# Kernel tuning notes

Hardware: AMD Instinct MI355X
Metric: run time of the kernel (lower is better)

Reference implementation:

```python
import jax, jax.numpy as jnp
import numpy as np
import math

B, S, E, H = 2, 2048, 1024, 16


def setup_inputs() -> dict:
    key = jax.random.key(0)
    ks = jax.random.split(key, 9)
    std = 0.02
    return {
        "x": jax.random.normal(ks[0], (B, S, E), dtype=jnp.float32),
        "Wq": jax.random.normal(ks[1], (E, E), dtype=jnp.float32) * std,
        "bq": jnp.zeros((E,), dtype=jnp.float32),
        "Wk": jax.random.normal(ks[2], (E, E), dtype=jnp.float32) * std,
        "bk": jnp.zeros((E,), dtype=jnp.float32),
        "Wv": jax.random.normal(ks[3], (E, E), dtype=jnp.float32) * std,
        "bv": jnp.zeros((E,), dtype=jnp.float32),
        "Wfc": jax.random.normal(ks[4], (E, E), dtype=jnp.float32) * std,
        "bfc": jnp.zeros((E,), dtype=jnp.float32),
        "n_head": H,
    }


def reference(x, Wq, bq, Wk, bk, Wv, bv, Wfc, bfc, n_head):
    Bn, Sn, En = x.shape
    Hd = En // n_head  # head_dim
    # torch Linear: y = x @ W.T + b
    def proj(W, b):
        return (x @ W.T + b).reshape(Bn, Sn, n_head, Hd).transpose(0, 2, 1, 3)  # [B,H,S,D]
    q = proj(Wq, bq)
    k = proj(Wk, bk)
    v = proj(Wv, bv)
    scores = jnp.einsum('bhqd,bhkd->bhqk', q, k) / math.sqrt(Hd)  # [B,H,S,S]
    # ALiBi: slopes_h = 2^{-(h+1)}; alibi[h,i,j] = -slope_h * (i - j)
    slopes = 2.0 ** (-jnp.arange(1, n_head + 1, dtype=jnp.float32))  # [H]
    pos = jnp.arange(Sn, dtype=jnp.float32)
    rel = pos[:, None] - pos[None, :]  # [S,S], memory_pos - context_pos
    alibi = -slopes[:, None, None] * rel  # [H,S,S]
    scores = scores + alibi[None]
    weights = jax.nn.softmax(scores, axis=-1)  # [B,H,S,S]
    out = jnp.einsum('bhqk,bhkd->bqhd', weights, v).reshape(Bn, Sn, En)
    out = out @ Wfc.T + bfc
    return (out, weights)
```

## Files before the change

### kernel.cpp

```cpp
#include <hip/hip_runtime.h>
#include <hip/hip_bf16.h>
#include <cstdint>
#include <cstddef>

#define BB 2
#define SS 2048
#define EE 1024
#define HH 16
#define MM (BB*SS)

typedef __bf16 bf16;
typedef __bf16 bf16x8 __attribute__((ext_vector_type(8)));
typedef float f32x4 __attribute__((ext_vector_type(4)));

#define GLD16(gsrc, ldst) \
  __builtin_amdgcn_global_load_lds((const __attribute__((address_space(1))) void*)(gsrc), \
                                   (__attribute__((address_space(3))) void*)(ldst), 16, 0, 0)

#define VMWAIT(N) do { asm volatile("s_waitcnt vmcnt(" #N ")" ::: "memory"); \
                       __builtin_amdgcn_sched_barrier(0); } while (0)
#define XBAR() do { __builtin_amdgcn_s_barrier(); \
                    __builtin_amdgcn_sched_barrier(0); } while (0)

__global__ __launch_bounds__(256) void cvt_f32_bf16(const float* __restrict__ src,
                                                    bf16* __restrict__ dst, int n) {
    int i = (blockIdx.x * 256 + threadIdx.x) * 8;
    if (i >= n) return;
    float4 a = *(const float4*)(src + i);
    float4 b = *(const float4*)(src + i + 4);
    bf16 o[8] = {(bf16)a.x,(bf16)a.y,(bf16)a.z,(bf16)a.w,
                 (bf16)b.x,(bf16)b.y,(bf16)b.z,(bf16)b.w};
    *(uint4*)(dst + i) = *(uint4*)o;
}

__global__ __launch_bounds__(256) void cvt4(const float* __restrict__ a, const float* __restrict__ b,
                                            const float* __restrict__ c, const float* __restrict__ d,
                                            bf16* __restrict__ oa, bf16* __restrict__ ob,
                                            bf16* __restrict__ oc, bf16* __restrict__ od) {
    int sel = blockIdx.y;
    const float* s = sel == 0 ? a : sel == 1 ? b : sel == 2 ? c : d;
    bf16* o       = sel == 0 ? oa : sel == 1 ? ob : sel == 2 ? oc : od;
    int i = (blockIdx.x * 256 + threadIdx.x) * 8;
    float4 x = *(const float4*)(s + i);
    float4 y = *(const float4*)(s + i + 4);
    bf16 t[8] = {(bf16)x.x,(bf16)x.y,(bf16)x.z,(bf16)x.w,
                 (bf16)y.x,(bf16)y.y,(bf16)y.z,(bf16)y.w};
    *(uint4*)(o + i) = *(uint4*)t;
}

template<int MODE>
__global__ __launch_bounds__(256) void gemm128(const bf16* __restrict__ A,
                                               const bf16* __restrict__ W0,
                                               const bf16* __restrict__ W1,
                                               const bf16* __restrict__ W2,
                                               const float* __restrict__ b0,
                                               const float* __restrict__ b1,
                                               const float* __restrict__ b2,
                                               void* __restrict__ o0,
                                               void* __restrict__ o1,
                                               void* __restrict__ o2) {
    __shared__ bf16 Al[128*64];
    __shared__ bf16 Bl[128*64];
    const int t = threadIdx.x;
    const int wsel = blockIdx.x >> 3;
    const int n0 = (blockIdx.x & 7) * 128;
    const int m0 = blockIdx.y * 128;
    const bf16* W  = wsel == 0 ? W0 : wsel == 1 ? W1 : W2;
    const float* bias = wsel == 0 ? b0 : wsel == 1 ? b1 : b2;
    void* outp = wsel == 0 ? o0 : wsel == 1 ? o1 : o2;

    const int w = t >> 6, lane = t & 63, lg = lane >> 4, li = lane & 15;
    const int wr = w >> 1, wc = w & 1;
    f32x4 acc[4][4] = {};

    for (int k0 = 0; k0 < 1024; k0 += 64) {
        __syncthreads();
        #pragma unroll
        for (int i = 0; i < 4; ++i) {
            int f = i * 256 + t;
            int row = f >> 3, c = (f & 7) * 8;
            GLD16(A + (size_t)(m0 + row) * 1024 + k0 + c, Al + f * 8);
            GLD16(W + (size_t)(n0 + row) * 1024 + k0 + c, Bl + f * 8);
        }
        __syncthreads();
        #pragma unroll
        for (int ks = 0; ks < 2; ++ks) {
            bf16x8 af[4], bf_[4];
            #pragma unroll
            for (int m = 0; m < 4; ++m)
                af[m] = *(const bf16x8*)&Al[(wr*64 + m*16 + li)*64 + ks*32 + lg*8];
            #pragma unroll
            for (int n = 0; n < 4; ++n)
                bf_[n] = *(const bf16x8*)&Bl[(wc*64 + n*16 + li)*64 + ks*32 + lg*8];
            #pragma unroll
            for (int m = 0; m < 4; ++m)
                #pragma unroll
                for (int n = 0; n < 4; ++n)
                    acc[m][n] = __builtin_amdgcn_mfma_f32_16x16x32_bf16(af[m], bf_[n], acc[m][n], 0,0,0);
        }
    }
    #pragma unroll
    for (int m = 0; m < 4; ++m)
      #pragma unroll
      for (int n = 0; n < 4; ++n)
        #pragma unroll
        for (int r = 0; r < 4; ++r) {
            int row = m0 + wr*64 + m*16 + lg*4 + r;
            int col = n0 + wc*64 + n*16 + li;
            float v = acc[m][n][r] + bias[col];
            if (MODE == 0) {
                int b = row >> 11, s = row & (SS-1);
                int h = col >> 6, d = col & 63;
                ((bf16*)outp)[(((size_t)(b*HH + h)*SS + s) << 6) + d] = (bf16)v;
            } else {
                ((float*)outp)[(size_t)row*1024 + col] = v;
            }
        }
}

__global__ __launch_bounds__(256) void transpose_v(const bf16* __restrict__ V,
                                                   bf16* __restrict__ Vt) {
    __shared__ bf16 L[64][72];
    const int bh = blockIdx.y, s0 = blockIdx.x * 64, t = threadIdx.x;
    for (int id = t; id < 512; id += 256) {
        int row = id >> 3, c = id & 7;
        *(uint4*)&L[row][c*8] = *(const uint4*)&V[((size_t)bh*SS + s0 + row)*64 + c*8];
    }
    __syncthreads();
    for (int id = t; id < 512; id += 256) {
        int d = id >> 3, c = id & 7;
        bf16 tmp[8];
        #pragma unroll
        for (int jj = 0; jj < 8; ++jj) tmp[jj] = L[c*8 + jj][d];
        *(uint4*)&Vt[((size_t)bh*64 + d)*SS + s0 + c*8] = *(uint4*)tmp;
    }
}

__global__ __launch_bounds__(256) void attn_kernel(const bf16* __restrict__ Q,
                                                   const bf16* __restrict__ Kk,
                                                   const bf16* __restrict__ Vt,
                                                   float* __restrict__ wout,
                                                   bf16* __restrict__ aout) {
    __shared__ bf16 ring[4][64*64];
    __shared__ float Lred[2][64];

    const int lin = blockIdx.x + (int)(gridDim.x * blockIdx.y);
    const int nl  = (lin & 7) * 128 + (lin >> 3);
    const int qt = nl & 31, bh = nl >> 5;

    const int b = bh >> 4, h = bh & 15;
    const int q0 = qt * 64;
    const int t = threadIdx.x, w = t >> 6, lane = t & 63, lg = lane >> 4, li = lane & 15;
    const int jh = w & 1, qh = w >> 1;
    const float slope = exp2f(-(float)(h + 1));
    const size_t kvbase = (size_t)bh * SS * 64;
    const size_t vtbase = (size_t)bh * 64 * SS;
    const float L2E = 1.4426950408889634f;
    const float K1 = 0.125f * L2E;
    const float C  = slope * L2E;
    const float C64 = C * 64.f;

    bf16x8 aq[2][2];
    #pragma unroll
    for (int cbq = 0; cbq < 2; ++cbq) {
        const bf16* qptr = Q + kvbase + (size_t)(q0 + qh*32 + cbq*16 + li) * 64;
        aq[cbq][0] = *(const bf16x8*)(qptr + lg*8);
        aq[cbq][1] = *(const bf16x8*)(qptr + 32 + lg*8);
    }

    const int swz = (li & 7) << 4;

    #define STAGE_K(J0, DST) do {                                              \
        _Pragma("unroll")                                                      \
        for (int i_ = 0; i_ < 2; ++i_) {                                       \
            int f_ = i_*256 + t; int row_ = f_ >> 3, c_ = f_ & 7;              \
            GLD16(Kk + kvbase + (size_t)((J0) + row_)*64 + (c_ ^ (row_ & 7))*8,\
                  (DST) + f_*8);                                               \
        } } while (0)
    #define STAGE_V(J0, DST) do {                                              \
        _Pragma("unroll")                                                      \
        for (int i_ = 0; i_ < 2; ++i_) {                                       \
            int f_ = i_*256 + t; int row_ = f_ >> 3, c_ = f_ & 7;              \
            GLD16(Vt + vtbase + (size_t)row_*SS + (J0) + (c_ ^ (row_ & 7))*8,  \
                  (DST) + f_*8);                                               \
        } } while (0)

    float cj[2][4];
    #pragma unroll
    for (int jt = 0; jt < 2; ++jt)
        #pragma unroll
        for (int r = 0; r < 4; ++r)
            cj[jt][r] = C * (float)(jh*32 + jt*16 + lg*4 + r - (SS-1));
    float lp[2] = {0.f, 0.f};

    STAGE_K(0,  &ring[0][0]);
    STAGE_K(64, &ring[1][0]);
    VMWAIT(2);
    XBAR();
    for (int kt = 0; kt < 32; ++kt) {
        if (kt + 2 < 32) STAGE_K((kt+2)*64, &ring[(kt+2) & 3][0]);
        const char* Ksb = (const char*)&ring[kt & 3][0];
        bf16x8 ak[2][2];
        #pragma unroll
        for (int jt = 0; jt < 2; ++jt) {
            int row = jh*32 + jt*16 + li;
            ak[jt][0] = *(const bf16x8*)(Ksb + row*128 + ((     lg*16) ^ swz));
            ak[jt][1] = *(const bf16x8*)(Ksb + row*128 + ((64 + lg*16) ^ swz));
        }
        f32x4 sc[2][2] = {};
        __builtin_amdgcn_s_setprio(1);
        #pragma unroll
        for (int jt = 0; jt < 2; ++jt)
            #pragma unroll
            for (int cbq = 0; cbq < 2; ++cbq) {
                sc[jt][cbq] = __builtin_amdgcn_mfma_f32_16x16x32_bf16(ak[jt][0], aq[cbq][0], sc[jt][cbq], 0,0,0);
                sc[jt][cbq] = __builtin_amdgcn_mfma_f32_16x16x32_bf16(ak[jt][1], aq[cbq][1], sc[jt][cbq], 0,0,0);
            }
        __builtin_amdgcn_s_setprio(0);
        #pragma unroll
        for (int jt = 0; jt < 2; ++jt) {
            #pragma unroll
            for (int cbq = 0; cbq < 2; ++cbq)
                #pragma unroll
                for (int r = 0; r < 4; ++r)
                    lp[cbq] += __builtin_amdgcn_exp2f(fmaf(sc[jt][cbq][r], K1, cj[jt][r]));
            #pragma unroll
            for (int r = 0; r < 4; ++r) cj[jt][r] += C64;
        }
        if (kt < 30) { VMWAIT(2); } else { VMWAIT(0); }
        XBAR();
    }
    #pragma unroll
    for (int cbq = 0; cbq < 2; ++cbq) {
        lp[cbq] += __shfl_xor(lp[cbq], 16);
        lp[cbq] += __shfl_xor(lp[cbq], 32);
    }
    if (lg == 0) {
        Lred[jh][qh*32 + li]      = lp[0];
        Lred[jh][qh*32 + 16 + li] = lp[1];
    }
    STAGE_K(0, &ring[0][0]);
    STAGE_V(0, &ring[2][0]);
    asm volatile("s_waitcnt vmcnt(0) lgkmcnt(0)" ::: "memory");
    __builtin_amdgcn_sched_barrier(0);
    XBAR();
    float lgl[2];
    #pragma unroll
    for (int cbq = 0; cbq < 2; ++cbq) {
        int qi = qh*32 + cbq*16 + li;
        lgl[cbq] = __builtin_amdgcn_logf(Lred[0][qi] + Lred[1][qi]);
    }
    float ecr[2][2][4];
    #pragma unroll
    for (int jt = 0; jt < 2; ++jt)
        #pragma unroll
        for (int cbq = 0; cbq < 2; ++cbq)
            #pragma unroll
            for (int r = 0; r < 4; ++r)
                ecr[jt][cbq][r] = C * (float)(jh*32 + jt*16 + lg*4 + r - (SS-1)) - lgl[cbq];

    f32x4 acc[2][4] = {};
    float* wrow0 = wout + ((size_t)bh*SS + q0 + qh*32 +      li) * SS;
    float* wrow1 = wout + ((size_t)bh*SS + q0 + qh*32 + 16 + li) * SS;

    for (int kt = 0; kt < 32; ++kt) {
        const int cur = kt & 1;
        const int j0 = kt * 64;
        if (kt + 1 < 32) {
            STAGE_K(j0 + 64, &ring[cur ^ 1][0]);
            STAGE_V(j0 + 64, &ring[2 + (cur ^ 1)][0]);
        }
        const char* Ksb = (const char*)&ring[cur][0];
        const char* Vsb = (const char*)&ring[2 + cur][0];
        bf16x8 ak[2][2];
        #pragma unroll
        for (int jt = 0; jt < 2; ++jt) {
            int row = jh*32 + jt*16 + li;
            ak[jt][0] = *(const bf16x8*)(Ksb + row*128 + ((     lg*16) ^ swz));
            ak[jt][1] = *(const bf16x8*)(Ksb + row*128 + ((64 + lg*16) ^ swz));
        }
        f32x4 sc[2][2] = {};
        __builtin_amdgcn_s_setprio(1);
        #pragma unroll
        for (int jt = 0; jt < 2; ++jt)
            #pragma unroll
            for (int cbq = 0; cbq < 2; ++cbq) {
                sc[jt][cbq] = __builtin_amdgcn_mfma_f32_16x16x32_bf16(ak[jt][0], aq[cbq][0], sc[jt][cbq], 0,0,0);
                sc[jt][cbq] = __builtin_amdgcn_mfma_f32_16x16x32_bf16(ak[jt][1], aq[cbq][1], sc[jt][cbq], 0,0,0);
            }
        __builtin_amdgcn_s_setprio(0);
        f32x4 wv[2][2];
        #pragma unroll
        for (int jt = 0; jt < 2; ++jt)
            #pragma unroll
            for (int cbq = 0; cbq < 2; ++cbq) {
                f32x4 v;
                v[0] = __builtin_amdgcn_exp2f(fmaf(sc[jt][cbq][0], K1, ecr[jt][cbq][0]));
                v[1] = __builtin_amdgcn_exp2f(fmaf(sc[jt][cbq][1], K1, ecr[jt][cbq][1]));
                v[2] = __builtin_amdgcn_exp2f(fmaf(sc[jt][cbq][2], K1, ecr[jt][cbq][2]));
                v[3] = __builtin_amdgcn_exp2f(fmaf(sc[jt][cbq][3], K1, ecr[jt][cbq][3]));
                wv[jt][cbq] = v;
                float* wr = (cbq == 0 ? wrow0 : wrow1);
                __builtin_nontemporal_store(v, (f32x4*)&wr[j0 + jh*32 + jt*16 + lg*4]);
                ecr[jt][cbq][0] += C64; ecr[jt][cbq][1] += C64;
                ecr[jt][cbq][2] += C64; ecr[jt][cbq][3] += C64;
            }
        bf16x8 pa[2];
        #pragma unroll
        for (int cbq = 0; cbq < 2; ++cbq) {
            bf16x8 p;
            p[0] = (bf16)wv[0][cbq][0]; p[1] = (bf16)wv[0][cbq][1];
            p[2] = (bf16)wv[0][cbq][2]; p[3] = (bf16)wv[0][cbq][3];
            p[4] = (bf16)wv[1][cbq][0]; p[5] = (bf16)wv[1][cbq][1];
            p[6] = (bf16)wv[1][cbq][2]; p[7] = (bf16)wv[1][cbq][3];
            pa[cbq] = p;
        }
        bf16x8 vb[4];
        #pragma unroll
        for (int d0 = 0; d0 < 4; ++d0) {
            int row = d0*16 + li;
            uint2 u0 = *(const uint2*)(Vsb + row*128 + ((jh*64      + lg*8) ^ swz));
            uint2 u1 = *(const uint2*)(Vsb + row*128 + ((jh*64 + 32 + lg*8) ^ swz));
            uint4 uu = {u0.x, u0.y, u1.x, u1.y};
            vb[d0] = __builtin_bit_cast(bf16x8, uu);
        }
        __builtin_amdgcn_s_setprio(1);
        #pragma unroll
        for (int cbq = 0; cbq < 2; ++cbq)
            #pragma unroll
            for (int d0 = 0; d0 < 4; ++d0)
                acc[cbq][d0] = __builtin_amdgcn_mfma_f32_16x16x32_bf16(pa[cbq], vb[d0], acc[cbq][d0], 0,0,0);
        __builtin_amdgcn_s_setprio(0);
        VMWAIT(4);
        XBAR();
    }

    bf16* Obuf = &ring[0][0];
    #pragma unroll
    for (int cbq = 0; cbq < 2; ++cbq)
        #pragma unroll
        for (int d0 = 0; d0 < 4; ++d0)
            #pragma unroll
            for (int r = 0; r < 4; ++r)
                Obuf[jh*4096 + (qh*32 + cbq*16 + lg*4 + r)*64 + d0*16 + li] =
                    (bf16)acc[cbq][d0][r];
    __syncthreads();
    {
        int q = t >> 2, dc = (t & 3) << 4;
        const bf16* o0 = Obuf +        q*64 + dc;
        const bf16* o1 = Obuf + 4096 + q*64 + dc;
        bf16x8 a0 = *(const bf16x8*)(o0),     a1 = *(const bf16x8*)(o0 + 8);
        bf16x8 b0 = *(const bf16x8*)(o1),     b1 = *(const bf16x8*)(o1 + 8);
        bf16 ov[16];
        #pragma unroll
        for (int e = 0; e < 8; ++e) {
            ov[e]     = (bf16)((float)a0[e] + (float)b0[e]);
            ov[8 + e] = (bf16)((float)a1[e] + (float)b1[e]);
        }
        bf16* dst = aout + ((size_t)(b*SS + q0 + q))*EE + h*64 + dc;
        *(uint4*)(dst)     = *(uint4*)(ov);
        *(uint4*)(dst + 8) = *(uint4*)(ov + 8);
    }
    #undef STAGE_K
    #undef STAGE_V
}

extern "C" void kernel_launch(void* const* d_in, const int* in_sizes, int n_in,
                              void* d_out, int out_size, void* d_ws, size_t ws_size,
                              hipStream_t stream) {
    const float* x   = (const float*)d_in[0];
    const float* Wq  = (const float*)d_in[1];
    const float* bq  = (const float*)d_in[2];
    const float* Wk  = (const float*)d_in[3];
    const float* bk  = (const float*)d_in[4];
    const float* Wv  = (const float*)d_in[5];
    const float* bv  = (const float*)d_in[6];
    const float* Wfc = (const float*)d_in[7];
    const float* bfc = (const float*)d_in[8];

    char* ws = (char*)d_ws;
    const size_t MB = 1024u*1024u;
    bf16* xb  = (bf16*)(ws + 0);
    bf16* wqb = (bf16*)(ws + 8*MB);
    bf16* wkb = (bf16*)(ws + 10*MB);
    bf16* wvb = (bf16*)(ws + 12*MB);
    bf16* wfb = (bf16*)(ws + 14*MB);
    bf16* Qb  = (bf16*)(ws + 16*MB);
    bf16* Kb  = (bf16*)(ws + 24*MB);
    bf16* Vb  = (bf16*)(ws + 32*MB);
    bf16* Vtb = (bf16*)(ws + 40*MB);
    bf16* Ab  = (bf16*)(ws + 48*MB);

    float* outp = (float*)d_out;
    float* wout = outp + (size_t)BB*SS*EE;

    cvt_f32_bf16<<<dim3(4194304/8/256), 256, 0, stream>>>(x, xb, 4194304);
    cvt4<<<dim3(512, 4), 256, 0, stream>>>(Wq, Wk, Wv, Wfc, wqb, wkb, wvb, wfb);

    gemm128<0><<<dim3(24, 32), 256, 0, stream>>>(xb, wqb, wkb, wvb, bq, bk, bv, Qb, Kb, Vb);

    transpose_v<<<dim3(SS/64, BB*HH), 256, 0, stream>>>(Vb, Vtb);

    attn_kernel<<<dim3(32, 32), 256, 0, stream>>>(Qb, Kb, Vtb, wout, Ab);

    gemm128<1><<<dim3(8, 32), 256, 0, stream>>>(Ab, wfb, wfb, wfb, bfc, bfc, bfc, d_out, d_out, d_out);
}
```

Baseline: 299.8 us.

## Split attention into PV pass with deferred normalization and separate weights-writing kernel

The single attention kernel did two passes over K: first to compute softmax denominators, then to compute normalized weights, store them and accumulate PV. Now attn1 does one pass that accumulates unnormalized PV together with the row sums, then rescales the output by the inverse sum and writes the log-sum to a workspace buffer. A new weights_kernel recomputes QK^T from global K, reads the log-sum and streams the normalized weights matrix, split over twice as many blocks. This removes the dedicated row-sum pass from the PV kernel but still recomputes QK^T for the weights output and adds a kernel launch. It also drops the custom vmcnt waits in favour of plain __syncthreads, and the log-sum buffer reuses the xb workspace region.

Result: slower. 341.4 us (+13.9%).

```diff
diff --git a/kernel.cpp b/kernel.cpp
--- a/kernel.cpp
+++ b/kernel.cpp
@@ -16,11 +16,6 @@
 #define GLD16(gsrc, ldst) \
   __builtin_amdgcn_global_load_lds((const __attribute__((address_space(1))) void*)(gsrc), \
                                    (__attribute__((address_space(3))) void*)(ldst), 16, 0, 0)
-
-#define VMWAIT(N) do { asm volatile("s_waitcnt vmcnt(" #N ")" ::: "memory"); \
-                       __builtin_amdgcn_sched_barrier(0); } while (0)
-#define XBAR() do { __builtin_amdgcn_s_barrier(); \
-                    __builtin_amdgcn_sched_barrier(0); } while (0)
 
 __global__ __launch_bounds__(256) void cvt_f32_bf16(const float* __restrict__ src,
                                                     bf16* __restrict__ dst, int n) {
@@ -136,11 +131,11 @@
     }
 }
 
-__global__ __launch_bounds__(256) void attn_kernel(const bf16* __restrict__ Q,
-                                                   const bf16* __restrict__ Kk,
-                                                   const bf16* __restrict__ Vt,
-                                                   float* __restrict__ wout,
-                                                   bf16* __restrict__ aout) {
+__global__ __launch_bounds__(256) void attn1_kernel(const bf16* __restrict__ Q,
+                                                    const bf16* __restrict__ Kk,
+                                                    const bf16* __restrict__ Vt,
+                                                    float* __restrict__ Lbuf,
+                                                    bf16* __restrict__ aout) {
     __shared__ bf16 ring[4][64*64];
     __shared__ float Lred[2][64];
 
@@ -167,7 +162,6 @@
         aq[cbq][0] = *(const bf16x8*)(qptr + lg*8);
         aq[cbq][1] = *(const bf16x8*)(qptr + 32 + lg*8);
     }
-
     const int swz = (li & 7) << 4;
 
     #define STAGE_K(J0, DST) do {                                              \
@@ -192,77 +186,11 @@
         for (int r = 0; r < 4; ++r)
             cj[jt][r] = C * (float)(jh*32 + jt*16 + lg*4 + r - (SS-1));
     float lp[2] = {0.f, 0.f};
-
-    STAGE_K(0,  &ring[0][0]);
-    STAGE_K(64, &ring[1][0]);
-    VMWAIT(2);
-    XBAR();
-    for (int kt = 0; kt < 32; ++kt) {
-        if (kt + 2 < 32) STAGE_K((kt+2)*64, &ring[(kt+2) & 3][0]);
-        const char* Ksb = (const char*)&ring[kt & 3][0];
-        bf16x8 ak[2][2];
-        #pragma unroll
-        for (int jt = 0; jt < 2; ++jt) {
-            int row = jh*32 + jt*16 + li;
-            ak[jt][0] = *(const bf16x8*)(Ksb + row*128 + ((     lg*16) ^ swz));
-            ak[jt][1] = *(const bf16x8*)(Ksb + row*128 + ((64 + lg*16) ^ swz));
-        }
-        f32x4 sc[2][2] = {};
-        __builtin_amdgcn_s_setprio(1);
-        #pragma unroll
-        for (int jt = 0; jt < 2; ++jt)
-            #pragma unroll
-            for (int cbq = 0; cbq < 2; ++cbq) {
-                sc[jt][cbq] = __builtin_amdgcn_mfma_f32_16x16x32_bf16(ak[jt][0], aq[cbq][0], sc[jt][cbq], 0,0,0);
-                sc[jt][cbq] = __builtin_amdgcn_mfma_f32_16x16x32_bf16(ak[jt][1], aq[cbq][1], sc[jt][cbq], 0,0,0);
-            }
-        __builtin_amdgcn_s_setprio(0);
-        #pragma unroll
-        for (int jt = 0; jt < 2; ++jt) {
-            #pragma unroll
-            for (int cbq = 0; cbq < 2; ++cbq)
-                #pragma unroll
-                for (int r = 0; r < 4; ++r)
-                    lp[cbq] += __builtin_amdgcn_exp2f(fmaf(sc[jt][cbq][r], K1, cj[jt][r]));
-            #pragma unroll
-            for (int r = 0; r < 4; ++r) cj[jt][r] += C64;
-        }
-        if (kt < 30) { VMWAIT(2); } else { VMWAIT(0); }
-        XBAR();
-    }
-    #pragma unroll
-    for (int cbq = 0; cbq < 2; ++cbq) {
-        lp[cbq] += __shfl_xor(lp[cbq], 16);
-        lp[cbq] += __shfl_xor(lp[cbq], 32);
-    }
-    if (lg == 0) {
-        Lred[jh][qh*32 + li]      = lp[0];
-        Lred[jh][qh*32 + 16 + li] = lp[1];
-    }
+    f32x4 acc[2][4] = {};
+
     STAGE_K(0, &ring[0][0]);
     STAGE_V(0, &ring[2][0]);
-    asm volatile("s_waitcnt vmcnt(0) lgkmcnt(0)" ::: "memory");
-    __builtin_amdgcn_sched_barrier(0);
-    XBAR();
-    float lgl[2];
-    #pragma unroll
-    for (int cbq = 0; cbq < 2; ++cbq) {
-        int qi = qh*32 + cbq*16 + li;
-        lgl[cbq] = __builtin_amdgcn_logf(Lred[0][qi] + Lred[1][qi]);
-    }
-    float ecr[2][2][4];
-    #pragma unroll
-    for (int jt = 0; jt < 2; ++jt)
-        #pragma unroll
-        for (int cbq = 0; cbq < 2; ++cbq)
-            #pragma unroll
-            for (int r = 0; r < 4; ++r)
-                ecr[jt][cbq][r] = C * (float)(jh*32 + jt*16 + lg*4 + r - (SS-1)) - lgl[cbq];
-
-    f32x4 acc[2][4] = {};
-    float* wrow0 = wout + ((size_t)bh*SS + q0 + qh*32 +      li) * SS;
-    float* wrow1 = wout + ((size_t)bh*SS + q0 + qh*32 + 16 + li) * SS;
-
+    __syncthreads();
     for (int kt = 0; kt < 32; ++kt) {
         const int cur = kt & 1;
         const int j0 = kt * 64;
@@ -291,20 +219,20 @@
         __builtin_amdgcn_s_setprio(0);
         f32x4 wv[2][2];
         #pragma unroll
-        for (int jt = 0; jt < 2; ++jt)
+        for (int jt = 0; jt < 2; ++jt) {
             #pragma unroll
             for (int cbq = 0; cbq < 2; ++cbq) {
                 f32x4 v;
-                v[0] = __builtin_amdgcn_exp2f(fmaf(sc[jt][cbq][0], K1, ecr[jt][cbq][0]));
-                v[1] = __builtin_amdgcn_exp2f(fmaf(sc[jt][cbq][1], K1, ecr[jt][cbq][1]));
-                v[2] = __builtin_amdgcn_exp2f(fmaf(sc[jt][cbq][2], K1, ecr[jt][cbq][2]));
-                v[3] = __builtin_amdgcn_exp2f(fmaf(sc[jt][cbq][3], K1, ecr[jt][cbq][3]));
+                #pragma unroll
+                for (int r = 0; r < 4; ++r) {
+                    v[r] = __builtin_amdgcn_exp2f(fmaf(sc[jt][cbq][r], K1, cj[jt][r]));
+                    lp[cbq] += v[r];
+                }
                 wv[jt][cbq] = v;
-                float* wr = (cbq == 0 ? wrow0 : wrow1);
-                __builtin_nontemporal_store(v, (f32x4*)&wr[j0 + jh*32 + jt*16 + lg*4]);
-                ecr[jt][cbq][0] += C64; ecr[jt][cbq][1] += C64;
-                ecr[jt][cbq][2] += C64; ecr[jt][cbq][3] += C64;
             }
+            #pragma unroll
+            for (int r = 0; r < 4; ++r) cj[jt][r] += C64;
+        }
         bf16x8 pa[2];
         #pragma unroll
         for (int cbq = 0; cbq < 2; ++cbq) {
@@ -331,9 +259,31 @@
             for (int d0 = 0; d0 < 4; ++d0)
                 acc[cbq][d0] = __builtin_amdgcn_mfma_f32_16x16x32_bf16(pa[cbq], vb[d0], acc[cbq][d0], 0,0,0);
         __builtin_amdgcn_s_setprio(0);
-        VMWAIT(4);
-        XBAR();
-    }
+        __syncthreads();
+    }
+    #pragma unroll
+    for (int cbq = 0; cbq < 2; ++cbq) {
+        lp[cbq] += __shfl_xor(lp[cbq], 16);
+        lp[cbq] += __shfl_xor(lp[cbq], 32);
+    }
+    if (lg == 0) {
+        Lred[jh][qh*32 + li]      = lp[0];
+        Lred[jh][qh*32 + 16 + li] = lp[1];
+    }
+    __syncthreads();
+    if (t < 64) {
+        float lv = Lred[0][t] + Lred[1][t];
+        Lbuf[(size_t)bh*SS + q0 + t] = __builtin_amdgcn_logf(lv);
+    }
+    float rinv2[2][4];
+    #pragma unroll
+    for (int cbq = 0; cbq < 2; ++cbq)
+        #pragma unroll
+        for (int r = 0; r < 4; ++r) {
+            int qi = qh*32 + cbq*16 + lg*4 + r;
+            rinv2[cbq][r] = 1.f / (Lred[0][qi] + Lred[1][qi]);
+        }
+    __syncthreads();
 
     bf16* Obuf = &ring[0][0];
     #pragma unroll
@@ -343,7 +293,7 @@
             #pragma unroll
             for (int r = 0; r < 4; ++r)
                 Obuf[jh*4096 + (qh*32 + cbq*16 + lg*4 + r)*64 + d0*16 + li] =
-                    (bf16)acc[cbq][d0][r];
+                    (bf16)(acc[cbq][d0][r] * rinv2[cbq][r]);
     __syncthreads();
     {
         int q = t >> 2, dc = (t & 3) << 4;
@@ -363,6 +313,84 @@
     }
     #undef STAGE_K
     #undef STAGE_V
+}
+
+__global__ __launch_bounds__(256) void weights_kernel(const bf16* __restrict__ Q,
+                                                      const bf16* __restrict__ Kk,
+                                                      const float* __restrict__ Lbuf,
+                                                      float* __restrict__ wout) {
+    const int lin = blockIdx.x + (int)(gridDim.x * blockIdx.y);
+    const int nl  = (lin & 7) * 256 + (lin >> 3);
+    const int bh = nl >> 6, rr = nl & 63;
+    const int qt = rr >> 1, jc = rr & 1;
+
+    const int h = bh & 15;
+    const int q0 = qt * 64;
+    const int jbase = jc * 1024;
+    const int t = threadIdx.x, w = t >> 6, lane = t & 63, lg = lane >> 4, li = lane & 15;
+    const int jh = w & 1, qh = w >> 1;
+    const float slope = exp2f(-(float)(h + 1));
+    const size_t kvbase = (size_t)bh * SS * 64;
+    const float L2E = 1.4426950408889634f;
+    const float K1 = 0.125f * L2E;
+    const float C  = slope * L2E;
+    const float C64 = C * 64.f;
+
+    bf16x8 aq[2][2];
+    float lgl[2];
+    #pragma unroll
+    for (int cbq = 0; cbq < 2; ++cbq) {
+        const int qi = q0 + qh*32 + cbq*16 + li;
+        const bf16* qptr = Q + kvbase + (size_t)qi * 64;
+        aq[cbq][0] = *(const bf16x8*)(qptr + lg*8);
+        aq[cbq][1] = *(const bf16x8*)(qptr + 32 + lg*8);
+        lgl[cbq] = Lbuf[(size_t)bh*SS + qi];
+    }
+    float ecr[2][2][4];
+    #pragma unroll
+    for (int jt = 0; jt < 2; ++jt)
+        #pragma unroll
+        for (int cbq = 0; cbq < 2; ++cbq)
+            #pragma unroll
+            for (int r = 0; r < 4; ++r)
+                ecr[jt][cbq][r] = C * (float)(jbase + jh*32 + jt*16 + lg*4 + r - (SS-1)) - lgl[cbq];
+
+    float* wrow0 = wout + ((size_t)bh*SS + q0 + qh*32 +      li) * SS;
+    float* wrow1 = wout + ((size_t)bh*SS + q0 + qh*32 + 16 + li) * SS;
+
+    #pragma unroll 2
+    for (int kt = 0; kt < 16; ++kt) {
+        const int j0 = jbase + kt * 64;
+        bf16x8 ak[2][2];
+        #pragma unroll
+        for (int jt = 0; jt < 2; ++jt) {
+            const bf16* kr = Kk + kvbase + (size_t)(j0 + jh*32 + jt*16 + li) * 64;
+            ak[jt][0] = *(const bf16x8*)(kr + lg*8);
+            ak[jt][1] = *(const bf16x8*)(kr + 32 + lg*8);
+        }
+        f32x4 sc[2][2] = {};
+        #pragma unroll
+        for (int jt = 0; jt < 2; ++jt)
+            #pragma unroll
+            for (int cbq = 0; cbq < 2; ++cbq) {
+                sc[jt][cbq] = __builtin_amdgcn_mfma_f32_16x16x32_bf16(ak[jt][0], aq[cbq][0], sc[jt][cbq], 0,0,0);
+                sc[jt][cbq] = __builtin_amdgcn_mfma_f32_16x16x32_bf16(ak[jt][1], aq[cbq][1], sc[jt][cbq], 0,0,0);
+            }
+        #pragma unroll
+        for (int jt = 0; jt < 2; ++jt)
+            #pragma unroll
+            for (int cbq = 0; cbq < 2; ++cbq) {
+                f32x4 v;
+                v[0] = __builtin_amdgcn_exp2f(fmaf(sc[jt][cbq][0], K1, ecr[jt][cbq][0]));
+                v[1] = __builtin_amdgcn_exp2f(fmaf(sc[jt][cbq][1], K1, ecr[jt][cbq][1]));
+                v[2] = __builtin_amdgcn_exp2f(fmaf(sc[jt][cbq][2], K1, ecr[jt][cbq][2]));
+                v[3] = __builtin_amdgcn_exp2f(fmaf(sc[jt][cbq][3], K1, ecr[jt][cbq][3]));
+                float* wr = (cbq == 0 ? wrow0 : wrow1);
+                __builtin_nontemporal_store(v, (f32x4*)&wr[j0 + jh*32 + jt*16 + lg*4]);
+                ecr[jt][cbq][0] += C64; ecr[jt][cbq][1] += C64;
+                ecr[jt][cbq][2] += C64; ecr[jt][cbq][3] += C64;
+            }
+    }
 }
 
 extern "C" void kernel_launch(void* const* d_in, const int* in_sizes, int n_in,
@@ -380,16 +408,17 @@
 
     char* ws = (char*)d_ws;
     const size_t MB = 1024u*1024u;
-    bf16* xb  = (bf16*)(ws + 0);
-    bf16* wqb = (bf16*)(ws + 8*MB);
-    bf16* wkb = (bf16*)(ws + 10*MB);
-    bf16* wvb = (bf16*)(ws + 12*MB);
-    bf16* wfb = (bf16*)(ws + 14*MB);
-    bf16* Qb  = (bf16*)(ws + 16*MB);
-    bf16* Kb  = (bf16*)(ws + 24*MB);
-    bf16* Vb  = (bf16*)(ws + 32*MB);
-    bf16* Vtb = (bf16*)(ws + 40*MB);
-    bf16* Ab  = (bf16*)(ws + 48*MB);
+    bf16* xb   = (bf16*)(ws + 0);
+    bf16* wqb  = (bf16*)(ws + 8*MB);
+    bf16* wkb  = (bf16*)(ws + 10*MB);
+    bf16* wvb  = (bf16*)(ws + 12*MB);
+    bf16* wfb  = (bf16*)(ws + 14*MB);
+    bf16* Qb   = (bf16*)(ws + 16*MB);
+    bf16* Kb   = (bf16*)(ws + 24*MB);
+    bf16* Vb   = (bf16*)(ws + 32*MB);
+    bf16* Vtb  = (bf16*)(ws + 40*MB);
+    bf16* Ab   = (bf16*)(ws + 48*MB);
+    float* Lb  = (float*)(ws + 0);
 
     float* outp = (float*)d_out;
     float* wout = outp + (size_t)BB*SS*EE;
@@ -401,7 +430,9 @@
 
     transpose_v<<<dim3(SS/64, BB*HH), 256, 0, stream>>>(Vb, Vtb);
 
-    attn_kernel<<<dim3(32, 32), 256, 0, stream>>>(Qb, Kb, Vtb, wout, Ab);
+    attn1_kernel<<<dim3(32, 32), 256, 0, stream>>>(Qb, Kb, Vtb, Lb, Ab);
+
+    weights_kernel<<<dim3(64, 32), 256, 0, stream>>>(Qb, Kb, Lb, wout);
 
     gemm128<1><<<dim3(8, 32), 256, 0, stream>>>(Ab, wfb, wfb, wfb, bfc, bfc, bfc, d_out, d_out, d_out);
 }
```
